# Optimization experiments

Hardware: AMD Instinct MI355X
Metric: run time of the kernel (lower is better)

Reference implementation:

```python
import jax, jax.numpy as jnp
import numpy as np

B = 4096
D = 256
TEMP = 0.5


def setup_inputs() -> dict:
    key = jax.random.key(0)
    k1, k2 = jax.random.split(key)
    x_i = jax.random.normal(k1, (B, D), dtype=jnp.float32)
    x_j = jax.random.normal(k2, (B, D), dtype=jnp.float32)
    return {"x_i": x_i, "x_j": x_j}


def reference(x_i, x_j):
    b = x_i.shape[0]
    # L2-normalize rows (F.normalize with default eps=1e-12)
    def l2norm(x):
        n = jnp.linalg.norm(x, axis=1, keepdims=True)
        return x / jnp.maximum(n, 1e-12)

    z = jnp.concatenate([l2norm(x_i), l2norm(x_j)], axis=0)  # [2B, D]
    # rows of z are unit-norm, so cosine similarity == dot product
    sim = z @ z.T  # [2B, 2B]

    # positives: diagonals at offsets +B and -B
    idx = jnp.arange(b)
    sim_ij = sim[idx, idx + b]
    sim_ji = sim[idx + b, idx]
    pos = jnp.concatenate([sim_ij, sim_ji], axis=0)  # [2B]

    nom = jnp.exp(pos / TEMP)
    neg_mask = 1.0 - jnp.eye(2 * b, dtype=sim.dtype)
    denom = jnp.sum(neg_mask * jnp.exp(sim / TEMP), axis=1)  # [2B]
    loss = jnp.sum(-jnp.log(nom / denom)) / (2 * b)
    return loss
```

## Files before the change

kernel.cpp:

```cpp
#include <hip/hip_runtime.h>

#define NB   4096
#define ND   256
#define N2B  8192
#define INV_T 2.0f

typedef __attribute__((ext_vector_type(8))) short bf16x8;
typedef __attribute__((ext_vector_type(4))) float f32x4;

__device__ __forceinline__ void gload_lds16(const void* g, void* l) {
  __builtin_amdgcn_global_load_lds(
      (const __attribute__((address_space(1))) void*)g,
      (__attribute__((address_space(3))) void*)l, 16, 0, 0);
}

__device__ __forceinline__ unsigned short f2b(float f) {
  unsigned int u = __float_as_uint(f);
  u = (u + 0x7fffu + ((u >> 16) & 1u)) >> 16;
  return (unsigned short)u;
}
__device__ __forceinline__ float b2f(unsigned short h) {
  return __uint_as_float(((unsigned int)h) << 16);
}

__global__ __launch_bounds__(256) void k_normalize(
    const float* __restrict__ xi, const float* __restrict__ xj,
    unsigned short* __restrict__ Z, float* __restrict__ rowsum,
    float* __restrict__ pos) {
  __shared__ float sh[2][256];
  int wave = threadIdx.x >> 6, lane = threadIdx.x & 63;
  int r = (int)blockIdx.x * 2 + (wave & 1);
  bool isJ = wave >= 2;
  const float* src = (isJ ? xj : xi) + (size_t)r * ND;
  int zrow = r + (isJ ? NB : 0);

  float4 v = *(const float4*)(src + lane * 4);
  float ss = v.x * v.x + v.y * v.y + v.z * v.z + v.w * v.w;
#pragma unroll
  for (int m = 1; m < 64; m <<= 1) ss += __shfl_xor(ss, m, 64);
  float scale = 1.0f / fmaxf(sqrtf(ss), 1e-12f);
  unsigned short h0 = f2b(v.x * scale), h1 = f2b(v.y * scale);
  unsigned short h2 = f2b(v.z * scale), h3 = f2b(v.w * scale);
  ushort4 st; st.x = h0; st.y = h1; st.z = h2; st.w = h3;
  *(ushort4*)(Z + (size_t)zrow * ND + lane * 4) = st;

  float f0 = b2f(h0), f1 = b2f(h1), f2 = b2f(h2), f3 = b2f(h3);
  float d = f0 * f0 + f1 * f1 + f2 * f2 + f3 * f3;
#pragma unroll
  for (int m = 1; m < 64; m <<= 1) d += __shfl_xor(d, m, 64);
  if (lane == 0) rowsum[zrow] = -__expf(d * INV_T);

  if (isJ) {
    float* s = sh[wave & 1] + lane * 4;
    s[0] = f0; s[1] = f1; s[2] = f2; s[3] = f3;
  }
  __syncthreads();
  if (!isJ) {
    const float* s = sh[wave] + lane * 4;
    float p = f0 * s[0] + f1 * s[1] + f2 * s[2] + f3 * s[3];
#pragma unroll
    for (int m = 1; m < 64; m <<= 1) p += __shfl_xor(p, m, 64);
    if (lane == 0) pos[r] = p;
  }
}

#define BK 64
__global__ __launch_bounds__(256) void k_gemm_exp(
    const unsigned short* __restrict__ Z, float* __restrict__ rowsum) {
  __shared__ alignas(16) unsigned short As[128 * BK];
  __shared__ alignas(16) unsigned short Bs[128 * BK];

  int tid = threadIdx.x;
  int wave = tid >> 6, lane = tid & 63;

  int k = (int)blockIdx.x;
  int tm = (int)((sqrtf(8.0f * (float)k + 1.0f) - 1.0f) * 0.5f);
  while ((tm + 1) * (tm + 2) / 2 <= k) ++tm;
  while (tm * (tm + 1) / 2 > k) --tm;
  int tn = k - tm * (tm + 1) / 2;

  int warp_m = wave & 1, warp_n = wave >> 1;
  int quad = lane >> 4, c16 = lane & 15;

  f32x4 acc[4][4] = {};

  const unsigned short* Ag = Z + (size_t)tm * 128 * ND;
  const unsigned short* Bg = Z + (size_t)tn * 128 * ND;

  int lr = lane >> 3;
  int cs = lane & 7;

  for (int s = 0; s < 4; ++s) {
    int k0 = s * BK;
#pragma unroll
    for (int call = 0; call < 4; ++call) {
      int r0 = wave * 32 + call * 8;
      int row = r0 + lr;
      int gc = cs ^ (row & 7);
      int goff = row * ND + k0 + gc * 8;
      gload_lds16(Ag + goff, &As[r0 * BK]);
      gload_lds16(Bg + goff, &Bs[r0 * BK]);
    }
    asm volatile("s_waitcnt vmcnt(0)" ::: "memory");
    __syncthreads();

#pragma unroll
    for (int t = 0; t < 2; ++t) {
      bf16x8 af[4], bfr[4];
      int c = t * 4 + quad;
#pragma unroll
      for (int mi = 0; mi < 4; ++mi) {
        int row = warp_m * 64 + mi * 16 + c16;
        af[mi] = *(const bf16x8*)&As[(row * 8 + (c ^ (row & 7))) * 8];
      }
#pragma unroll
      for (int ni = 0; ni < 4; ++ni) {
        int row = warp_n * 64 + ni * 16 + c16;
        bfr[ni] = *(const bf16x8*)&Bs[(row * 8 + (c ^ (row & 7))) * 8];
      }
#pragma unroll
      for (int mi = 0; mi < 4; ++mi)
#pragma unroll
        for (int ni = 0; ni < 4; ++ni)
          acc[mi][ni] = __builtin_amdgcn_mfma_f32_16x16x32_bf16(
              af[mi], bfr[ni], acc[mi][ni], 0, 0, 0);
    }
    __syncthreads();
  }

  bool off = (tm != tn);
  float rs[4][4];
  float cs4[4] = {0.f, 0.f, 0.f, 0.f};
#pragma unroll
  for (int mi = 0; mi < 4; ++mi)
#pragma unroll
    for (int r = 0; r < 4; ++r) rs[mi][r] = 0.0f;
#pragma unroll
  for (int mi = 0; mi < 4; ++mi)
#pragma unroll
    for (int ni = 0; ni < 4; ++ni)
#pragma unroll
      for (int r = 0; r < 4; ++r) {
        float e = __expf(acc[mi][ni][r] * INV_T);
        rs[mi][r] += e;
        cs4[ni] += e;
      }

#pragma unroll
  for (int m = 1; m <= 8; m <<= 1)
#pragma unroll
    for (int mi = 0; mi < 4; ++mi)
#pragma unroll
      for (int r = 0; r < 4; ++r)
        rs[mi][r] += __shfl_xor(rs[mi][r], m, 64);

  int rowbase = tm * 128 + warp_m * 64;
#pragma unroll
  for (int mi = 0; mi < 4; ++mi)
#pragma unroll
    for (int r = 0; r < 4; ++r)
      if (c16 == mi * 4 + r)
        atomicAdd(&rowsum[rowbase + mi * 16 + quad * 4 + r], rs[mi][r]);

  if (off) {
#pragma unroll
    for (int m = 16; m <= 32; m <<= 1)
#pragma unroll
      for (int ni = 0; ni < 4; ++ni)
        cs4[ni] += __shfl_xor(cs4[ni], m, 64);
    if (quad == 0) {
      int colbase = tn * 128 + warp_n * 64;
#pragma unroll
      for (int ni = 0; ni < 4; ++ni)
        atomicAdd(&rowsum[colbase + ni * 16 + c16], cs4[ni]);
    }
  }
}

__global__ __launch_bounds__(1024) void k_final(
    const float* __restrict__ rowsum, const float* __restrict__ pos,
    float* __restrict__ out) {
  __shared__ float red[16];
  int tid = threadIdx.x;
  int wave = tid >> 6, lane = tid & 63;
  float acc = 0.0f;
#pragma unroll
  for (int t = 0; t < N2B / 1024; ++t) {
    int r = tid + t * 1024;
    acc += __logf(rowsum[r]) - INV_T * pos[r & (NB - 1)];
  }
#pragma unroll
  for (int m = 1; m < 64; m <<= 1) acc += __shfl_xor(acc, m, 64);
  if (lane == 0) red[wave] = acc;
  __syncthreads();
  if (tid == 0) {
    float t = 0.0f;
#pragma unroll
    for (int w = 0; w < 16; ++w) t += red[w];
    out[0] = t * (1.0f / (float)N2B);
  }
}

extern "C" void kernel_launch(void* const* d_in, const int* in_sizes, int n_in,
                              void* d_out, int out_size, void* d_ws,
                              size_t ws_size, hipStream_t stream) {
  const float* xi = (const float*)d_in[0];
  const float* xj = (const float*)d_in[1];
  float* out = (float*)d_out;
  char* ws = (char*)d_ws;
  unsigned short* Z = (unsigned short*)ws;
  float* rowsum = (float*)(ws + 4194304);
  float* pos = (float*)(ws + 4194304 + 32768);

  k_normalize<<<dim3(NB / 2), dim3(256), 0, stream>>>(xi, xj, Z, rowsum, pos);
  k_gemm_exp<<<dim3(64 * 65 / 2), dim3(256), 0, stream>>>(Z, rowsum);
  k_final<<<dim3(1), dim3(1024), 0, stream>>>(rowsum, pos, out);
}
```

Before: 112.0 us.

## Replace rowsum atomics with partial-sum buffer and parallel final reduction

```diff
diff --git a/kernel.cpp b/kernel.cpp
--- a/kernel.cpp
+++ b/kernel.cpp
@@ -25,9 +25,11 @@
 
 __global__ __launch_bounds__(256) void k_normalize(
     const float* __restrict__ xi, const float* __restrict__ xj,
-    unsigned short* __restrict__ Z, float* __restrict__ rowsum,
-    float* __restrict__ pos) {
+    unsigned short* __restrict__ Z, float* __restrict__ diagE,
+    float* __restrict__ pos, float* __restrict__ lossAcc,
+    unsigned int* __restrict__ ticket) {
   __shared__ float sh[2][256];
+  if (blockIdx.x == 0 && threadIdx.x == 0) { *lossAcc = 0.0f; *ticket = 0u; }
   int wave = threadIdx.x >> 6, lane = threadIdx.x & 63;
   int r = (int)blockIdx.x * 2 + (wave & 1);
   bool isJ = wave >= 2;
@@ -48,7 +50,7 @@
   float d = f0 * f0 + f1 * f1 + f2 * f2 + f3 * f3;
 #pragma unroll
   for (int m = 1; m < 64; m <<= 1) d += __shfl_xor(d, m, 64);
-  if (lane == 0) rowsum[zrow] = -__expf(d * INV_T);
+  if (lane == 0) diagE[zrow] = __expf(d * INV_T);
 
   if (isJ) {
     float* s = sh[wave & 1] + lane * 4;
@@ -66,7 +68,7 @@
 
 #define BK 64
 __global__ __launch_bounds__(256) void k_gemm_exp(
-    const unsigned short* __restrict__ Z, float* __restrict__ rowsum) {
+    const unsigned short* __restrict__ Z, float* __restrict__ R) {
   __shared__ alignas(16) unsigned short As[128 * BK];
   __shared__ alignas(16) unsigned short Bs[128 * BK];
 
@@ -155,12 +157,13 @@
         rs[mi][r] += __shfl_xor(rs[mi][r], m, 64);
 
   int rowbase = tm * 128 + warp_m * 64;
+  int rslot = tn * 2 + warp_n;
 #pragma unroll
   for (int mi = 0; mi < 4; ++mi)
 #pragma unroll
     for (int r = 0; r < 4; ++r)
       if (c16 == mi * 4 + r)
-        atomicAdd(&rowsum[rowbase + mi * 16 + quad * 4 + r], rs[mi][r]);
+        R[(size_t)(rowbase + mi * 16 + quad * 4 + r) * 128 + rslot] = rs[mi][r];
 
   if (off) {
 #pragma unroll
@@ -170,34 +173,47 @@
         cs4[ni] += __shfl_xor(cs4[ni], m, 64);
     if (quad == 0) {
       int colbase = tn * 128 + warp_n * 64;
+      int cslot = tm * 2 + warp_m;
 #pragma unroll
       for (int ni = 0; ni < 4; ++ni)
-        atomicAdd(&rowsum[colbase + ni * 16 + c16], cs4[ni]);
-    }
-  }
-}
-
-__global__ __launch_bounds__(1024) void k_final(
-    const float* __restrict__ rowsum, const float* __restrict__ pos,
-    float* __restrict__ out) {
-  __shared__ float red[16];
+        R[(size_t)(colbase + ni * 16 + c16) * 128 + cslot] = cs4[ni];
+    }
+  }
+}
+
+__global__ __launch_bounds__(256) void k_final(
+    const float* __restrict__ R, const float* __restrict__ diagE,
+    const float* __restrict__ pos, float* __restrict__ lossAcc,
+    unsigned int* __restrict__ ticket, float* __restrict__ out) {
+  __shared__ float red[4];
   int tid = threadIdx.x;
   int wave = tid >> 6, lane = tid & 63;
-  float acc = 0.0f;
-#pragma unroll
-  for (int t = 0; t < N2B / 1024; ++t) {
-    int r = tid + t * 1024;
-    acc += __logf(rowsum[r]) - INV_T * pos[r & (NB - 1)];
-  }
-#pragma unroll
-  for (int m = 1; m < 64; m <<= 1) acc += __shfl_xor(acc, m, 64);
-  if (lane == 0) red[wave] = acc;
+  int row = (int)blockIdx.x * 64 + (tid >> 2);
+  int c0 = (tid & 3) * 32;
+
+  const float* Rr = R + (size_t)row * 128 + c0;
+  float s = 0.0f;
+#pragma unroll
+  for (int i = 0; i < 8; ++i) {
+    float4 v = *(const float4*)(Rr + i * 4);
+    s += v.x + v.y + v.z + v.w;
+  }
+  s += __shfl_xor(s, 1, 64);
+  s += __shfl_xor(s, 2, 64);
+  float term = (__logf(s - diagE[row]) - INV_T * pos[row & (NB - 1)]) * 0.25f;
+#pragma unroll
+  for (int m = 1; m < 64; m <<= 1) term += __shfl_xor(term, m, 64);
+  if (lane == 0) red[wave] = term;
   __syncthreads();
   if (tid == 0) {
-    float t = 0.0f;
-#pragma unroll
-    for (int w = 0; w < 16; ++w) t += red[w];
-    out[0] = t * (1.0f / (float)N2B);
+    float bs = red[0] + red[1] + red[2] + red[3];
+    atomicAdd(lossAcc, bs);
+    __threadfence();
+    unsigned int old = atomicAdd(ticket, 1u);
+    if (old == 127u) {
+      float v = atomicAdd(lossAcc, 0.0f);
+      out[0] = v * (1.0f / (float)N2B);
+    }
   }
 }
 
@@ -209,10 +225,15 @@
   float* out = (float*)d_out;
   char* ws = (char*)d_ws;
   unsigned short* Z = (unsigned short*)ws;
-  float* rowsum = (float*)(ws + 4194304);
-  float* pos = (float*)(ws + 4194304 + 32768);
-
-  k_normalize<<<dim3(NB / 2), dim3(256), 0, stream>>>(xi, xj, Z, rowsum, pos);
-  k_gemm_exp<<<dim3(64 * 65 / 2), dim3(256), 0, stream>>>(Z, rowsum);
-  k_final<<<dim3(1), dim3(1024), 0, stream>>>(rowsum, pos, out);
-}
+  float* R = (float*)(ws + (4u << 20));
+  float* pos = (float*)(ws + (8u << 20));
+  float* diagE = (float*)(ws + (8u << 20) + 65536);
+  float* lossAcc = (float*)(ws + (8u << 20) + 131072);
+  unsigned int* ticket = (unsigned int*)(ws + (8u << 20) + 131072 + 64);
+
+  k_normalize<<<dim3(NB / 2), dim3(256), 0, stream>>>(xi, xj, Z, diagE, pos,
+                                                      lossAcc, ticket);
+  k_gemm_exp<<<dim3(64 * 65 / 2), dim3(256), 0, stream>>>(Z, R);
+  k_final<<<dim3(128), dim3(256), 0, stream>>>(R, diagE, pos, lossAcc, ticket,
+                                               out);
+}
```

Result: faster. 103.3 us (-7.7%).
